# Kernel tuning notes

Measured on AMD Instinct MI355X. Metric: run time of the kernel, lower is better.

Reference implementation:

```python
import jax, jax.numpy as jnp
import numpy as np

NUM_NETS = 2_000_000
PINS_PER_NET = 4
NUM_PINS = NUM_NETS * PINS_PER_NET


def setup_inputs() -> dict:
    key = jax.random.key(0)
    k1, k2, k3 = jax.random.split(key, 3)
    num_slrX, num_slrY = 1, 4
    # pin positions already expressed in SLR-grid units: x in [0, num_slrX), y in [0, num_slrY)
    pos = jax.random.uniform(k1, (NUM_PINS, 2), jnp.float32) * jnp.array(
        [float(max(num_slrX, 1)), float(max(num_slrY, 1))], jnp.float32)
    # CSR netpin structure: each net owns PINS_PER_NET pins, flat list is a permutation of all pins
    flat_netpin = jax.random.permutation(k2, NUM_PINS).astype(jnp.int32)
    netpin_start = (jnp.arange(NUM_NETS + 1, dtype=jnp.int32) * PINS_PER_NET)
    net_ids = jnp.repeat(jnp.arange(NUM_NETS, dtype=jnp.int32), PINS_PER_NET)
    net_weights = jax.random.uniform(k3, (NUM_NETS,), jnp.float32, minval=0.5, maxval=1.5)
    net_mask = jnp.ones((NUM_NETS,), jnp.bool_)
    pin_mask = jnp.zeros((NUM_PINS,), jnp.bool_)
    inv_gamma = jnp.float32(2.0)  # 1 / gamma, gamma = 0.5
    return dict(pos=pos, flat_netpin=flat_netpin, netpin_start=netpin_start,
                net_ids=net_ids, net_weights=net_weights, net_mask=net_mask,
                pin_mask=pin_mask, inv_gamma=inv_gamma,
                num_slrX=num_slrX, num_slrY=num_slrY)


def reference(pos, flat_netpin, netpin_start, net_ids, net_weights, net_mask,
              pin_mask, inv_gamma, num_slrX, num_slrY):
    """Weighted-average SLL: per-net log-sum-exp weighted-average span of pin
    SLR coordinates, per dimension, counted only for dims with >1 SLR."""
    n = net_weights.shape[0]
    p = pos[flat_netpin]  # [P, 2] gather pin coords in CSR order
    # numerically-stable exp weights per net (segment max/min shift)
    mx = jax.ops.segment_max(p, net_ids, num_segments=n)  # [N, 2]
    mn = jax.ops.segment_min(p, net_ids, num_segments=n)  # [N, 2]
    ep = jnp.exp((p - mx[net_ids]) * inv_gamma)   # exp(+x/gamma), shifted
    en = jnp.exp((mn[net_ids] - p) * inv_gamma)   # exp(-x/gamma), shifted
    s_ep = jax.ops.segment_sum(ep, net_ids, num_segments=n)
    s_xep = jax.ops.segment_sum(p * ep, net_ids, num_segments=n)
    s_en = jax.ops.segment_sum(en, net_ids, num_segments=n)
    s_xen = jax.ops.segment_sum(p * en, net_ids, num_segments=n)
    wa = s_xep / s_ep - s_xen / s_en  # [N, 2] weighted-average span per dim
    dim_on = jnp.array([num_slrX > 1, num_slrY > 1], dtype=wa.dtype)  # only multi-SLR dims
    per_net = jnp.sum(wa * dim_on, axis=1)  # [N]
    return jnp.sum(jnp.where(net_mask, net_weights * per_net, jnp.float32(0.0)))
```

## Files before the change

### kernel.cpp

```cpp
#include <hip/hip_runtime.h>
#include <stdint.h>


#define PINB_SHIFT 13
#define PINB_SIZE  (1 << PINB_SHIFT)
#define MAX_PINB   1024
#define JB_SHIFT   14
#define JB_SIZE    (1 << JB_SHIFT)
#define MAX_JB     512
#define P1_CHUNK   8192
#define P2_CHUNK   4096

__device__ __forceinline__ float wa4(float a, float b, float c, float d, float ig) {
    float ea = __expf(a * ig), eb = __expf(b * ig);
    float ec = __expf(c * ig), ed = __expf(d * ig);
    float na = __expf(-a * ig), nb = __expf(-b * ig);
    float nc = __expf(-c * ig), nd = __expf(-d * ig);
    float s_ep  = ea + eb + ec + ed;
    float s_xep = a * ea + b * eb + c * ec + d * ed;
    float s_en  = na + nb + nc + nd;
    float s_xen = a * na + b * nb + c * nc + d * nd;
    return s_xep / s_ep - s_xen / s_en;
}

__global__ void init_kernel(unsigned* __restrict__ cur1, int n_pinb,
                            unsigned* __restrict__ cur2, int n_jb,
                            float* __restrict__ out) {
    int t = threadIdx.x;
    if (t == 0) out[0] = 0.0f;
    for (int i = t; i < n_pinb; i += blockDim.x) cur1[i] = (unsigned)i << PINB_SHIFT;
    for (int i = t; i < n_jb;   i += blockDim.x) cur2[i] = (unsigned)i << JB_SHIFT;
}

__global__ void reinit_cur2_kernel(unsigned* __restrict__ cur2, int n_jb) {
    int t = threadIdx.x;
    for (int i = t; i < n_jb; i += blockDim.x) cur2[i] = (unsigned)i << JB_SHIFT;
}

__global__ __launch_bounds__(512) void p1_partition(
    const int4* __restrict__ fnp4, int NP, int n_pinb,
    uint2* __restrict__ ent1, unsigned* __restrict__ cur1)
{
    __shared__ uint2    staged[P1_CHUNK];
    __shared__ unsigned hist[MAX_PINB];
    __shared__ unsigned scn[MAX_PINB];
    __shared__ unsigned gbase[MAX_PINB];
    const int base  = blockIdx.x * P1_CHUNK;
    const int valid = min(P1_CHUNK, NP - base);
    const int t = threadIdx.x;

    for (int b = t; b < MAX_PINB; b += 512) hist[b] = 0;
    __syncthreads();

    unsigned pin[16], rnk[16];
    #pragma unroll
    for (int m4 = 0; m4 < 4; ++m4) {
        int k4 = t + 512 * m4;
        int kk = 4 * k4;
        int4 v = make_int4(0, 0, 0, 0);
        if (kk < valid) v = fnp4[(base >> 2) + k4];
        pin[4*m4+0] = (unsigned)v.x; pin[4*m4+1] = (unsigned)v.y;
        pin[4*m4+2] = (unsigned)v.z; pin[4*m4+3] = (unsigned)v.w;
    }
    #pragma unroll
    for (int m4 = 0; m4 < 4; ++m4)
        #pragma unroll
        for (int c = 0; c < 4; ++c) {
            int kk = 4 * (t + 512 * m4) + c;
            rnk[4*m4+c] = 0;
            if (kk < valid)
                rnk[4*m4+c] = atomicAdd(&hist[pin[4*m4+c] >> PINB_SHIFT], 1u);
        }
    __syncthreads();

    if (t < 64) {
        unsigned v[16], s = 0;
        #pragma unroll
        for (int i = 0; i < 16; ++i) { v[i] = hist[t * 16 + i]; s += v[i]; }
        unsigned e = s;
        #pragma unroll
        for (int off = 1; off < 64; off <<= 1) {
            unsigned u = __shfl_up(e, off, 64);
            if (t >= off) e += u;
        }
        e -= s;
        #pragma unroll
        for (int i = 0; i < 16; ++i) { scn[t * 16 + i] = e; e += v[i]; }
    }
    __syncthreads();
    for (int b = t; b < n_pinb; b += 512)
        if (hist[b]) gbase[b] = atomicAdd(&cur1[b], hist[b]);
    __syncthreads();

    #pragma unroll
    for (int m4 = 0; m4 < 4; ++m4)
        #pragma unroll
        for (int c = 0; c < 4; ++c) {
            int kk = 4 * (t + 512 * m4) + c;
            if (kk < valid) {
                unsigned p = pin[4*m4+c];
                staged[scn[p >> PINB_SHIFT] + rnk[4*m4+c]] =
                    make_uint2(p, (unsigned)(base + kk));
            }
        }
    __syncthreads();

    for (int k = t; k < valid; k += 512) {
        uint2 e = staged[k];
        unsigned b = e.x >> PINB_SHIFT;
        ent1[gbase[b] + ((unsigned)k - scn[b])] = e;
    }
}

__global__ __launch_bounds__(512) void p2_gather(
    const uint2* __restrict__ ent1, const float2* __restrict__ pos2,
    const int* __restrict__ slrx_p, const int* __restrict__ slry_p,
    int d, int NP, int n_jb,
    uint2* __restrict__ ent2, unsigned* __restrict__ cur2)
{
    const int slr = (d == 0) ? slrx_p[0] : slry_p[0];
    if (slr <= 1) return;

    __shared__ float    win[PINB_SIZE];
    __shared__ uint2    staged[P2_CHUNK];
    __shared__ unsigned hist[MAX_JB], scn[MAX_JB], gbase[MAX_JB];
    const int b       = blockIdx.x;
    const int pbase   = b << PINB_SHIFT;
    const int count_b = min(PINB_SIZE, NP - pbase);
    const int t = threadIdx.x;

    for (int i = t; i < count_b; i += 512) {
        float2 p = pos2[pbase + i];
        win[i] = d ? p.y : p.x;
    }

    #pragma unroll
    for (int r = 0; r < PINB_SIZE / P2_CHUNK; ++r) {
        const int cbase = r * P2_CHUNK;
        const int valid = min(P2_CHUNK, count_b - cbase);
        __syncthreads();
        for (int q = t; q < MAX_JB; q += 512) hist[q] = 0;
        __syncthreads();

        uint2 e[8]; unsigned rnk[8]; float yv[8];
        #pragma unroll
        for (int m = 0; m < 8; ++m) {
            int k = t + 512 * m;
            e[m] = make_uint2(0u, 0u);
            if (k < valid) e[m] = ent1[pbase + cbase + k];
        }
        #pragma unroll
        for (int m = 0; m < 8; ++m) {
            int k = t + 512 * m;
            yv[m] = (k < valid) ? win[e[m].x - (unsigned)pbase] : 0.0f;
        }
        #pragma unroll
        for (int m = 0; m < 8; ++m) {
            int k = t + 512 * m;
            rnk[m] = 0;
            if (k < valid) rnk[m] = atomicAdd(&hist[e[m].y >> JB_SHIFT], 1u);
        }
        __syncthreads();

        if (t < 64) {
            unsigned v[8], s = 0;
            #pragma unroll
            for (int i = 0; i < 8; ++i) { v[i] = hist[t * 8 + i]; s += v[i]; }
            unsigned ex = s;
            #pragma unroll
            for (int off = 1; off < 64; off <<= 1) {
                unsigned u = __shfl_up(ex, off, 64);
                if (t >= off) ex += u;
            }
            ex -= s;
            #pragma unroll
            for (int i = 0; i < 8; ++i) { scn[t * 8 + i] = ex; ex += v[i]; }
        }
        __syncthreads();
        if (t < n_jb && hist[t]) gbase[t] = atomicAdd(&cur2[t], hist[t]);
        __syncthreads();

        #pragma unroll
        for (int m = 0; m < 8; ++m) {
            int k = t + 512 * m;
            if (k < valid)
                staged[scn[e[m].y >> JB_SHIFT] + rnk[m]] =
                    make_uint2(e[m].y, __float_as_uint(yv[m]));
        }
        __syncthreads();

        for (int k = t; k < valid; k += 512) {
            uint2 s2 = staged[k];
            unsigned jb = s2.x >> JB_SHIFT;
            ent2[gbase[jb] + ((unsigned)k - scn[jb])] = s2;
        }
    }
}

__global__ __launch_bounds__(512) void p3_compute(
    const uint2* __restrict__ ent2, const float* __restrict__ wts,
    const float* __restrict__ ig_p,
    const int* __restrict__ slrx_p, const int* __restrict__ slry_p,
    int d, int NP, float* __restrict__ out)
{
    const int slr = (d == 0) ? slrx_p[0] : slry_p[0];
    if (slr <= 1) return;

    __shared__ float ytmp[JB_SIZE];
    const int jb     = blockIdx.x;
    const int base_j = jb << JB_SHIFT;
    const int nslots = min(JB_SIZE, NP - base_j);
    const int t = threadIdx.x;
    const float ig = ig_p[0];

    for (int k = t; k < nslots; k += 512) {
        uint2 e = ent2[base_j + k];
        ytmp[e.x & (JB_SIZE - 1)] = __uint_as_float(e.y);
    }
    __syncthreads();

    float val = 0.0f;
    const int nnets = nslots >> 2, bnet = base_j >> 2;
    const float4* y4 = (const float4*)ytmp;
    for (int i = t; i < nnets; i += 512) {
        float4 p = y4[i];
        val += wts[bnet + i] * wa4(p.x, p.y, p.z, p.w, ig);
    }

    #pragma unroll
    for (int off = 32; off > 0; off >>= 1) val += __shfl_down(val, off, 64);
    __syncthreads();
    if ((t & 63) == 0) ytmp[t >> 6] = val;
    __syncthreads();
    if (t == 0) {
        float s = 0.0f;
        #pragma unroll
        for (int w = 0; w < 8; ++w) s += ytmp[w];
        atomicAdd(out, s);
    }
}

__global__ __launch_bounds__(256) void wasll_fallback(
    const float2* __restrict__ pos, const int4* __restrict__ fnp4,
    const float* __restrict__ net_weights, const float* __restrict__ inv_gamma_p,
    const int* __restrict__ slrx_p, const int* __restrict__ slry_p,
    float* __restrict__ out, int num_nets)
{
    const float ig = inv_gamma_p[0];
    const float dx = (slrx_p[0] > 1) ? 1.0f : 0.0f;
    const float dy = (slry_p[0] > 1) ? 1.0f : 0.0f;
    int net = blockIdx.x * blockDim.x + threadIdx.x;
    float val = 0.0f;
    if (net < num_nets) {
        int4 idx = fnp4[net];
        float2 p0 = pos[idx.x], p1 = pos[idx.y], p2 = pos[idx.z], p3 = pos[idx.w];
        val = net_weights[net] * (dx * wa4(p0.x, p1.x, p2.x, p3.x, ig)
                                + dy * wa4(p0.y, p1.y, p2.y, p3.y, ig));
    }
    #pragma unroll
    for (int off = 32; off > 0; off >>= 1) val += __shfl_down(val, off, 64);
    __shared__ float smem[4];
    if ((threadIdx.x & 63) == 0) smem[threadIdx.x >> 6] = val;
    __syncthreads();
    if (threadIdx.x == 0)
        atomicAdd(out, smem[0] + smem[1] + smem[2] + smem[3]);
}

__global__ void zero_out_kernel(float* __restrict__ out) { out[0] = 0.0f; }

extern "C" void kernel_launch(void* const* d_in, const int* in_sizes, int n_in,
                              void* d_out, int out_size, void* d_ws, size_t ws_size,
                              hipStream_t stream) {
    const float* posf        = (const float*)d_in[0];
    const int*   fnp         = (const int*)d_in[1];
    const float* net_weights = (const float*)d_in[4];
    const float* inv_gamma   = (const float*)d_in[7];
    const int*   slrx        = (const int*)d_in[8];
    const int*   slry        = (const int*)d_in[9];
    float*       out         = (float*)d_out;
    const int    N  = in_sizes[4];
    const int    NP = in_sizes[1];

    const int n_pinb = (NP + PINB_SIZE - 1) >> PINB_SHIFT;
    const int n_jb   = (NP + JB_SIZE - 1) >> JB_SHIFT;

    size_t off = 0;
    auto carve = [&](size_t bytes) { size_t o = off; off += (bytes + 255) & ~size_t(255); return o; };
    size_t o_ent1 = carve((size_t)n_pinb * PINB_SIZE * sizeof(uint2));
    size_t o_ent2 = carve((size_t)n_jb * JB_SIZE * sizeof(uint2));
    size_t o_cur1 = carve((size_t)n_pinb * sizeof(unsigned));
    size_t o_cur2 = carve((size_t)n_jb * sizeof(unsigned));

    const bool ok = (NP == 4 * N) && (NP % 4 == 0) &&
                    (n_pinb <= MAX_PINB) && (n_jb <= MAX_JB) && (off <= ws_size);
    if (!ok) {
        hipLaunchKernelGGL(zero_out_kernel, dim3(1), dim3(1), 0, stream, out);
        const int block = 256, grid = (N + block - 1) / block;
        hipLaunchKernelGGL(wasll_fallback, dim3(grid), dim3(block), 0, stream,
                           (const float2*)posf, (const int4*)fnp, net_weights,
                           inv_gamma, slrx, slry, out, N);
        return;
    }

    char* ws = (char*)d_ws;
    uint2*    ent1 = (uint2*)(ws + o_ent1);
    uint2*    ent2 = (uint2*)(ws + o_ent2);
    unsigned* cur1 = (unsigned*)(ws + o_cur1);
    unsigned* cur2 = (unsigned*)(ws + o_cur2);

    hipLaunchKernelGGL(init_kernel, dim3(1), dim3(1024), 0, stream,
                       cur1, n_pinb, cur2, n_jb, out);

    const int g1 = (NP + P1_CHUNK - 1) / P1_CHUNK;
    hipLaunchKernelGGL(p1_partition, dim3(g1), dim3(512), 0, stream,
                       (const int4*)fnp, NP, n_pinb, ent1, cur1);

    hipLaunchKernelGGL(p2_gather, dim3(n_pinb), dim3(512), 0, stream,
                       ent1, (const float2*)posf, slrx, slry, 0, NP, n_jb, ent2, cur2);
    hipLaunchKernelGGL(p3_compute, dim3(n_jb), dim3(512), 0, stream,
                       ent2, net_weights, inv_gamma, slrx, slry, 0, NP, out);

    hipLaunchKernelGGL(reinit_cur2_kernel, dim3(1), dim3(1024), 0, stream, cur2, n_jb);

    hipLaunchKernelGGL(p2_gather, dim3(n_pinb), dim3(512), 0, stream,
                       ent1, (const float2*)posf, slrx, slry, 1, NP, n_jb, ent2, cur2);
    hipLaunchKernelGGL(p3_compute, dim3(n_jb), dim3(512), 0, stream,
                       ent2, net_weights, inv_gamma, slrx, slry, 1, NP, out);
}
```

Before: 278.3 us.

## Pack p2 entries as quantized 18-bit coordinates with slot index

Intermediate ent2 entries are packed into a single 32-bit word: a 14-bit slot index and an 18-bit fixed-point quantized coordinate, in place of an 8-byte index/float pair. This halves the scatter write and the p3 read traffic. The change also halves the p1/p2 chunk sizes, double-buffers the histogram so the zeroing barrier goes away, and folds the global base minus the scan offset into the histogram array so one lookup is saved per element. Quantizing coordinates to 18 bits adds rounding error in the exp-weighted spans, which is a real accuracy trade-off.

Result: slower. 311.8 us (+12.1%).

```diff
diff --git a/kernel.cpp b/kernel.cpp
--- a/kernel.cpp
+++ b/kernel.cpp
@@ -8,8 +8,11 @@
 #define JB_SHIFT   14
 #define JB_SIZE    (1 << JB_SHIFT)
 #define MAX_JB     512
-#define P1_CHUNK   8192
-#define P2_CHUNK   4096
+#define P1_CHUNK   4096
+#define P2_CHUNK   2048
+#define YQ_SHIFT   18
+#define YQ_ONE     262144.0f
+#define YQ_MASK    ((1u << YQ_SHIFT) - 1u)
 
 __device__ __forceinline__ float wa4(float a, float b, float c, float d, float ig) {
     float ea = __expf(a * ig), eb = __expf(b * ig);
@@ -44,7 +47,6 @@
     __shared__ uint2    staged[P1_CHUNK];
     __shared__ unsigned hist[MAX_PINB];
     __shared__ unsigned scn[MAX_PINB];
-    __shared__ unsigned gbase[MAX_PINB];
     const int base  = blockIdx.x * P1_CHUNK;
     const int valid = min(P1_CHUNK, NP - base);
     const int t = threadIdx.x;
@@ -52,25 +54,21 @@
     for (int b = t; b < MAX_PINB; b += 512) hist[b] = 0;
     __syncthreads();
 
-    unsigned pin[16], rnk[16];
-    #pragma unroll
-    for (int m4 = 0; m4 < 4; ++m4) {
+    unsigned pin[8], rnk[8];
+    #pragma unroll
+    for (int m4 = 0; m4 < 2; ++m4) {
         int k4 = t + 512 * m4;
-        int kk = 4 * k4;
         int4 v = make_int4(0, 0, 0, 0);
-        if (kk < valid) v = fnp4[(base >> 2) + k4];
+        if (4 * k4 < valid) v = fnp4[(base >> 2) + k4];
         pin[4*m4+0] = (unsigned)v.x; pin[4*m4+1] = (unsigned)v.y;
         pin[4*m4+2] = (unsigned)v.z; pin[4*m4+3] = (unsigned)v.w;
     }
     #pragma unroll
-    for (int m4 = 0; m4 < 4; ++m4)
-        #pragma unroll
-        for (int c = 0; c < 4; ++c) {
-            int kk = 4 * (t + 512 * m4) + c;
-            rnk[4*m4+c] = 0;
-            if (kk < valid)
-                rnk[4*m4+c] = atomicAdd(&hist[pin[4*m4+c] >> PINB_SHIFT], 1u);
-        }
+    for (int m = 0; m < 8; ++m) {
+        int kk = 4 * (t + 512 * (m >> 2)) + (m & 3);
+        rnk[m] = 0;
+        if (kk < valid) rnk[m] = atomicAdd(&hist[pin[m] >> PINB_SHIFT], 1u);
+    }
     __syncthreads();
 
     if (t < 64) {
@@ -88,27 +86,23 @@
         for (int i = 0; i < 16; ++i) { scn[t * 16 + i] = e; e += v[i]; }
     }
     __syncthreads();
-    for (int b = t; b < n_pinb; b += 512)
-        if (hist[b]) gbase[b] = atomicAdd(&cur1[b], hist[b]);
-    __syncthreads();
-
-    #pragma unroll
-    for (int m4 = 0; m4 < 4; ++m4)
-        #pragma unroll
-        for (int c = 0; c < 4; ++c) {
-            int kk = 4 * (t + 512 * m4) + c;
-            if (kk < valid) {
-                unsigned p = pin[4*m4+c];
-                staged[scn[p >> PINB_SHIFT] + rnk[4*m4+c]] =
-                    make_uint2(p, (unsigned)(base + kk));
-            }
-        }
+
+    for (int b = t; b < n_pinb; b += 512) {
+        unsigned h = hist[b];
+        hist[b] = (h ? atomicAdd(&cur1[b], h) : 0u) - scn[b];
+    }
+    #pragma unroll
+    for (int m = 0; m < 8; ++m) {
+        int kk = 4 * (t + 512 * (m >> 2)) + (m & 3);
+        if (kk < valid)
+            staged[scn[pin[m] >> PINB_SHIFT] + rnk[m]] =
+                make_uint2(pin[m], (unsigned)(base + kk));
+    }
     __syncthreads();
 
     for (int k = t; k < valid; k += 512) {
         uint2 e = staged[k];
-        unsigned b = e.x >> PINB_SHIFT;
-        ent1[gbase[b] + ((unsigned)k - scn[b])] = e;
+        ent1[hist[e.x >> PINB_SHIFT] + (unsigned)k] = e;
     }
 }
 
@@ -116,16 +110,18 @@
     const uint2* __restrict__ ent1, const float2* __restrict__ pos2,
     const int* __restrict__ slrx_p, const int* __restrict__ slry_p,
     int d, int NP, int n_jb,
-    uint2* __restrict__ ent2, unsigned* __restrict__ cur2)
+    unsigned* __restrict__ ent2, unsigned* __restrict__ cur2)
 {
     const int slr = (d == 0) ? slrx_p[0] : slry_p[0];
     if (slr <= 1) return;
-
-    __shared__ float    win[PINB_SIZE];
-    __shared__ uint2    staged[P2_CHUNK];
-    __shared__ unsigned hist[MAX_JB], scn[MAX_JB], gbase[MAX_JB];
-    const int b       = blockIdx.x;
-    const int pbase   = b << PINB_SHIFT;
+    const float qs = YQ_ONE / (float)slr;
+
+    __shared__ float          win[PINB_SIZE];
+    __shared__ unsigned       stagedP[P2_CHUNK];
+    __shared__ unsigned short stagedJ[P2_CHUNK];
+    __shared__ unsigned       hist[2][MAX_JB];
+    __shared__ unsigned       scn[MAX_JB];
+    const int pbase   = blockIdx.x << PINB_SHIFT;
     const int count_b = min(PINB_SIZE, NP - pbase);
     const int t = threadIdx.x;
 
@@ -133,39 +129,43 @@
         float2 p = pos2[pbase + i];
         win[i] = d ? p.y : p.x;
     }
+    for (int q = t; q < MAX_JB; q += 512) hist[0][q] = 0;
 
     #pragma unroll
     for (int r = 0; r < PINB_SIZE / P2_CHUNK; ++r) {
+        unsigned* cur = hist[r & 1];
+        unsigned* nxt = hist[(r + 1) & 1];
         const int cbase = r * P2_CHUNK;
         const int valid = min(P2_CHUNK, count_b - cbase);
+
         __syncthreads();
-        for (int q = t; q < MAX_JB; q += 512) hist[q] = 0;
-        __syncthreads();
-
-        uint2 e[8]; unsigned rnk[8]; float yv[8];
-        #pragma unroll
-        for (int m = 0; m < 8; ++m) {
+        for (int q = t; q < MAX_JB; q += 512) nxt[q] = 0;
+
+        uint2 e[4]; unsigned rnk[4], jb[4], pk[4];
+        #pragma unroll
+        for (int m = 0; m < 4; ++m) {
             int k = t + 512 * m;
-            e[m] = make_uint2(0u, 0u);
-            if (k < valid) e[m] = ent1[pbase + cbase + k];
-        }
-        #pragma unroll
-        for (int m = 0; m < 8; ++m) {
+            e[m] = (k < valid) ? ent1[pbase + cbase + k] : make_uint2(0u, 0u);
+        }
+        #pragma unroll
+        for (int m = 0; m < 4; ++m) {
             int k = t + 512 * m;
-            yv[m] = (k < valid) ? win[e[m].x - (unsigned)pbase] : 0.0f;
-        }
-        #pragma unroll
-        for (int m = 0; m < 8; ++m) {
+            float y = (k < valid) ? win[e[m].x - (unsigned)pbase] : 0.0f;
+            unsigned yq = min((unsigned)(y * qs + 0.5f), YQ_MASK);
+            jb[m] = e[m].y >> JB_SHIFT;
+            pk[m] = ((e[m].y & (JB_SIZE - 1u)) << YQ_SHIFT) | yq;
+        }
+        #pragma unroll
+        for (int m = 0; m < 4; ++m) {
             int k = t + 512 * m;
-            rnk[m] = 0;
-            if (k < valid) rnk[m] = atomicAdd(&hist[e[m].y >> JB_SHIFT], 1u);
+            rnk[m] = (k < valid) ? atomicAdd(&cur[jb[m]], 1u) : 0u;
         }
         __syncthreads();
 
         if (t < 64) {
             unsigned v[8], s = 0;
             #pragma unroll
-            for (int i = 0; i < 8; ++i) { v[i] = hist[t * 8 + i]; s += v[i]; }
+            for (int i = 0; i < 8; ++i) { v[i] = cur[t * 8 + i]; s += v[i]; }
             unsigned ex = s;
             #pragma unroll
             for (int off = 1; off < 64; off <<= 1) {
@@ -177,45 +177,48 @@
             for (int i = 0; i < 8; ++i) { scn[t * 8 + i] = ex; ex += v[i]; }
         }
         __syncthreads();
-        if (t < n_jb && hist[t]) gbase[t] = atomicAdd(&cur2[t], hist[t]);
+
+        if (t < n_jb) {
+            unsigned h = cur[t];
+            cur[t] = (h ? atomicAdd(&cur2[t], h) : 0u) - scn[t];
+        }
+        #pragma unroll
+        for (int m = 0; m < 4; ++m) {
+            int k = t + 512 * m;
+            if (k < valid) {
+                unsigned pos = scn[jb[m]] + rnk[m];
+                stagedP[pos] = pk[m];
+                stagedJ[pos] = (unsigned short)jb[m];
+            }
+        }
         __syncthreads();
 
-        #pragma unroll
-        for (int m = 0; m < 8; ++m) {
-            int k = t + 512 * m;
-            if (k < valid)
-                staged[scn[e[m].y >> JB_SHIFT] + rnk[m]] =
-                    make_uint2(e[m].y, __float_as_uint(yv[m]));
-        }
-        __syncthreads();
-
         for (int k = t; k < valid; k += 512) {
-            uint2 s2 = staged[k];
-            unsigned jb = s2.x >> JB_SHIFT;
-            ent2[gbase[jb] + ((unsigned)k - scn[jb])] = s2;
+            unsigned jbk = stagedJ[k];
+            ent2[cur[jbk] + (unsigned)k] = stagedP[k];
         }
     }
 }
 
 __global__ __launch_bounds__(512) void p3_compute(
-    const uint2* __restrict__ ent2, const float* __restrict__ wts,
+    const unsigned* __restrict__ ent2, const float* __restrict__ wts,
     const float* __restrict__ ig_p,
     const int* __restrict__ slrx_p, const int* __restrict__ slry_p,
     int d, int NP, float* __restrict__ out)
 {
     const int slr = (d == 0) ? slrx_p[0] : slry_p[0];
     if (slr <= 1) return;
+    const float dq = (float)slr / YQ_ONE;
 
     __shared__ float ytmp[JB_SIZE];
-    const int jb     = blockIdx.x;
-    const int base_j = jb << JB_SHIFT;
+    const int base_j = blockIdx.x << JB_SHIFT;
     const int nslots = min(JB_SIZE, NP - base_j);
     const int t = threadIdx.x;
     const float ig = ig_p[0];
 
     for (int k = t; k < nslots; k += 512) {
-        uint2 e = ent2[base_j + k];
-        ytmp[e.x & (JB_SIZE - 1)] = __uint_as_float(e.y);
+        unsigned e = ent2[base_j + k];
+        ytmp[e >> YQ_SHIFT] = (float)(e & YQ_MASK) * dq;
     }
     __syncthreads();
 
@@ -287,7 +290,7 @@
     size_t off = 0;
     auto carve = [&](size_t bytes) { size_t o = off; off += (bytes + 255) & ~size_t(255); return o; };
     size_t o_ent1 = carve((size_t)n_pinb * PINB_SIZE * sizeof(uint2));
-    size_t o_ent2 = carve((size_t)n_jb * JB_SIZE * sizeof(uint2));
+    size_t o_ent2 = carve((size_t)n_jb * JB_SIZE * sizeof(unsigned));
     size_t o_cur1 = carve((size_t)n_pinb * sizeof(unsigned));
     size_t o_cur2 = carve((size_t)n_jb * sizeof(unsigned));
 
@@ -304,7 +307,7 @@
 
     char* ws = (char*)d_ws;
     uint2*    ent1 = (uint2*)(ws + o_ent1);
-    uint2*    ent2 = (uint2*)(ws + o_ent2);
+    unsigned* ent2 = (unsigned*)(ws + o_ent2);
     unsigned* cur1 = (unsigned*)(ws + o_cur1);
     unsigned* cur2 = (unsigned*)(ws + o_cur2);
 
```
